# Kernel tuning notes

Hardware: AMD Instinct MI355X
Metric: run time of the kernel (lower is better)

The kernel has to match this reference:

```python
import jax, jax.numpy as jnp
import numpy as np

B, T, C = 4, 128, 512
NH, HS = 8, 64          # n_head, head_dim = C // NH
ORDER = 3               # attention_order
SCALE = 1.0 / np.sqrt(HS)


def setup_inputs() -> dict:
    key = jax.random.key(0)
    ks = jax.random.split(key, 7)
    s = 0.02
    return {
        "x": jax.random.normal(ks[0], (B, T, C), jnp.float32),
        "Wp0": jax.random.normal(ks[1], (C, C), jnp.float32) * s,
        "Wp1": jax.random.normal(ks[2], (C, C), jnp.float32) * s,
        "Wp2": jax.random.normal(ks[3], (C, C), jnp.float32) * s,
        "Wv0": jax.random.normal(ks[4], (HS, HS), jnp.float32) * s,
        "Wv1": jax.random.normal(ks[5], (HS, HS), jnp.float32) * s,
        "Wc": jax.random.normal(ks[6], (C, C), jnp.float32) * s,
    }


def _heads(x, W):
    # Linear then split heads: (B,T,C) -> (B,NH,T,HS)
    return (x @ W).reshape(B, T, NH, HS).transpose(0, 2, 1, 3)


def _causal_mask(t, order):
    # indices grid [T]^order, True where i0 >= i1 >= ... >= i_{order-1}
    idx = jnp.arange(t)
    g = jnp.stack(jnp.meshgrid(*([idx] * order), indexing='ij'), axis=-1)
    return jnp.all(jnp.diff(g, axis=-1) <= 0, axis=-1)


def reference(x, Wp0, Wp1, Wp2, Wv0, Wv1, Wc):
    p0 = _heads(x, Wp0)  # (B,NH,T,HS)
    p1 = _heads(x, Wp1)
    p2 = _heads(x, Wp2)

    # pairwise scores, then higher-order broadcast exactly as the torch einsum
    # ('bh...i,bhkd->bh...ik' sums the key over d and broadcasts — faithful).
    att = jnp.einsum('bhid,bhjd->bhij', p0, p1) * SCALE        # (B,NH,T,T)
    att = jnp.einsum('bh...i,bhkd->bh...ik', att, p2)          # (B,NH,T,T,T)

    mask = _causal_mask(T, ORDER)[None, None]                  # (1,1,T,T,T)
    att = jnp.where(mask, att, -jnp.inf)
    att = jax.nn.softmax(att.reshape(B, NH, T, T * T), axis=-1)

    # value tensors with broadcasted elementwise product over the order dims
    V0 = (p1 @ Wv0)[:, :, :, None, :]   # (B,NH,T,1,HS)
    V1 = (p2 @ Wv1)[:, :, None, :, :]   # (B,NH,1,T,HS)
    V = (V0 * V1).reshape(B, NH, T * T, HS)

    y = jnp.einsum('bhij,bhjd->bhid', att, V)                  # (B,NH,T,HS)
    y = y.transpose(0, 2, 1, 3).reshape(B, T, C)
    return y @ Wc
```

## Files before the change

### kernel.cpp

```cpp
#include <hip/hip_runtime.h>
#include <hip/hip_bf16.h>
#include <math.h>

#define B 4
#define T 128
#define C 512
#define NH 8
#define HS 64
#define BH (B*NH)

typedef __attribute__((ext_vector_type(8))) short bf16x8;
typedef __attribute__((ext_vector_type(4))) float f32x4;

__device__ __forceinline__ unsigned short bfc(float x) {
    return __builtin_bit_cast(unsigned short, __float2bfloat16(x));
}
__device__ __forceinline__ float b2f(unsigned short u) {
    unsigned int x = ((unsigned int)u) << 16;
    return __builtin_bit_cast(float, x);
}
__device__ __forceinline__ unsigned int pk_bf16(float a, float b) {
    return (unsigned int)bfc(a) | ((unsigned int)bfc(b) << 16);
}
__device__ __forceinline__ float lo_f(unsigned int g) {
    return __builtin_bit_cast(float, g << 16);
}
__device__ __forceinline__ float hi_f(unsigned int g) {
    return __builtin_bit_cast(float, g & 0xffff0000u);
}

__global__ __launch_bounds__(256) void prep_kernel(
    const float* __restrict__ X, const float* __restrict__ Wp0, const float* __restrict__ Wp1,
    const float* __restrict__ Wp2, const float* __restrict__ Wc,
    const float* __restrict__ Wv0, const float* __restrict__ Wv1,
    unsigned short* __restrict__ Xb, unsigned short* __restrict__ W0T, unsigned short* __restrict__ W1T,
    unsigned short* __restrict__ W2T, unsigned short* __restrict__ WcT,
    unsigned short* __restrict__ We0T, unsigned short* __restrict__ We1T)
{
    __shared__ float Ls[64][69];
    __shared__ float As[16][68];
    __shared__ float Bs[16][68];
    const int z = blockIdx.z;
    const int tid = threadIdx.x;
    if (z == 0) {
        const int r0 = blockIdx.y * 64, c0 = blockIdx.x * 64;
        #pragma unroll
        for (int it = 0; it < 2; ++it) {
            const int q = tid + it * 256;
            const int row = q >> 3, c8 = (q & 7) * 8;
            const float4 a = *(const float4*)&X[(size_t)(r0 + row) * 512 + c0 + c8];
            const float4 b = *(const float4*)&X[(size_t)(r0 + row) * 512 + c0 + c8 + 4];
            uint4 o;
            o.x = pk_bf16(a.x, a.y);
            o.y = pk_bf16(a.z, a.w);
            o.z = pk_bf16(b.x, b.y);
            o.w = pk_bf16(b.z, b.w);
            *(uint4*)&Xb[(size_t)(r0 + row) * 512 + c0 + c8] = o;
        }
        return;
    }
    if (z <= 4) {
        const int r0 = blockIdx.y * 64, c0 = blockIdx.x * 64;
        const float* W = (z == 1) ? Wp0 : (z == 2) ? Wp1 : (z == 3) ? Wp2 : Wc;
        unsigned short* WT = (z == 1) ? W0T : (z == 2) ? W1T : (z == 3) ? W2T : WcT;
        #pragma unroll
        for (int it = 0; it < 4; ++it) {
            const int q = tid + it * 256;
            const int row = q >> 4, c4 = (q & 15) * 4;
            const float4 v = *(const float4*)&W[(size_t)(r0 + row) * 512 + c0 + c4];
            Ls[row][c4 + 0] = v.x; Ls[row][c4 + 1] = v.y; Ls[row][c4 + 2] = v.z; Ls[row][c4 + 3] = v.w;
        }
        __syncthreads();
        #pragma unroll
        for (int it = 0; it < 2; ++it) {
            const int q = tid + it * 256;
            const int nrow = q >> 3, k8 = (q & 7) * 8;
            uint4 o;
            o.x = pk_bf16(Ls[k8 + 0][nrow], Ls[k8 + 1][nrow]);
            o.y = pk_bf16(Ls[k8 + 2][nrow], Ls[k8 + 3][nrow]);
            o.z = pk_bf16(Ls[k8 + 4][nrow], Ls[k8 + 5][nrow]);
            o.w = pk_bf16(Ls[k8 + 6][nrow], Ls[k8 + 7][nrow]);
            *(uint4*)&WT[(size_t)(c0 + nrow) * 512 + r0 + k8] = o;
        }
        return;
    }
    const float* A  = (z == 5) ? Wp1 : Wp2;
    const float* Wv = (z == 5) ? Wv0 : Wv1;
    unsigned short* O = (z == 5) ? We0T : We1T;
    const int h = blockIdx.x;
    const int m0 = blockIdx.y * 64;
    const int tx = tid & 15, ty = tid >> 4;
    const int arow = tid >> 2, acol = (tid & 3) * 4;
    const int brow = tid >> 4, bcol = (tid & 15) * 4;
    float acc[4][4] = {};
    for (int k0 = 0; k0 < 64; k0 += 16) {
        const float4 av = *(const float4*)&A[(size_t)(m0 + arow) * 512 + h * 64 + k0 + acol];
        const float4 bv = *(const float4*)&Wv[(size_t)(k0 + brow) * 64 + bcol];
        __syncthreads();
        As[acol + 0][arow] = av.x; As[acol + 1][arow] = av.y;
        As[acol + 2][arow] = av.z; As[acol + 3][arow] = av.w;
        *(float4*)&Bs[brow][bcol] = bv;
        __syncthreads();
        #pragma unroll
        for (int kk = 0; kk < 16; ++kk) {
            const float4 a4 = *(const float4*)&As[kk][ty * 4];
            const float4 b4 = *(const float4*)&Bs[kk][tx * 4];
            const float ar[4] = {a4.x, a4.y, a4.z, a4.w};
            const float br[4] = {b4.x, b4.y, b4.z, b4.w};
            #pragma unroll
            for (int r = 0; r < 4; ++r)
                #pragma unroll
                for (int c = 0; c < 4; ++c)
                    acc[r][c] = fmaf(ar[r], br[c], acc[r][c]);
        }
    }
    #pragma unroll
    for (int r = 0; r < 4; ++r)
        #pragma unroll
        for (int c = 0; c < 4; ++c)
            O[(size_t)(h * 64 + tx * 4 + c) * 512 + (m0 + ty * 4 + r)] = bfc(acc[r][c]);
}

__global__ __launch_bounds__(256) void projmm_kernel(
    const unsigned short* __restrict__ Xb,
    const unsigned short* __restrict__ W0T, const unsigned short* __restrict__ W1T,
    const unsigned short* __restrict__ W2T,
    const unsigned short* __restrict__ We0T, const unsigned short* __restrict__ We1T,
    unsigned short* __restrict__ p0b, unsigned short* __restrict__ p1b,
    unsigned short* __restrict__ V0T, unsigned short* __restrict__ V1T, float* __restrict__ rr)
{
    __shared__ __align__(16) unsigned short As[64][72];
    __shared__ __align__(16) unsigned short Bs[64][72];
    __shared__ float sRS[4][64];
    const int z = blockIdx.z;
    const unsigned short* WT = (z == 0) ? W0T : (z == 1) ? W1T : (z == 2) ? W2T : (z == 3) ? We0T : We1T;
    const int m0 = blockIdx.y * 64, n0 = blockIdx.x * 64;
    const int tid = threadIdx.x;
    const int w = tid >> 6, lane = tid & 63, quad = lane >> 4, l16 = lane & 15;
    f32x4 acc[4];
    #pragma unroll
    for (int mt = 0; mt < 4; ++mt) acc[mt] = (f32x4){0.f, 0.f, 0.f, 0.f};
    for (int k0 = 0; k0 < 512; k0 += 64) {
        __syncthreads();
        #pragma unroll
        for (int it = 0; it < 2; ++it) {
            const int q = tid + it * 256;
            const int row = q >> 3, c8 = (q & 7) * 8;
            *(uint4*)&As[row][c8] = *(const uint4*)&Xb[(size_t)(m0 + row) * 512 + k0 + c8];
            *(uint4*)&Bs[row][c8] = *(const uint4*)&WT[(size_t)(n0 + row) * 512 + k0 + c8];
        }
        __syncthreads();
        #pragma unroll
        for (int kt = 0; kt < 2; ++kt) {
            const bf16x8 b8 = *(const bf16x8*)&Bs[w * 16 + l16][kt * 32 + quad * 8];
            #pragma unroll
            for (int mt = 0; mt < 4; ++mt) {
                const bf16x8 a8 = *(const bf16x8*)&As[mt * 16 + l16][kt * 32 + quad * 8];
                acc[mt] = __builtin_amdgcn_mfma_f32_16x16x32_bf16(a8, b8, acc[mt], 0, 0, 0);
            }
        }
    }
    if (z == 2) {
        #pragma unroll
        for (int mt = 0; mt < 4; ++mt)
            #pragma unroll
            for (int r = 0; r < 4; ++r) {
                float v = acc[mt][r];
                v += __shfl_xor(v, 1, 64); v += __shfl_xor(v, 2, 64);
                v += __shfl_xor(v, 4, 64); v += __shfl_xor(v, 8, 64);
                if (l16 == 0) sRS[w][mt * 16 + quad * 4 + r] = v;
            }
        __syncthreads();
        if (tid < 64) {
            const float s = sRS[0][tid] + sRS[1][tid] + sRS[2][tid] + sRS[3][tid];
            const int m = m0 + tid, b = m >> 7, tl = m & 127, h = n0 >> 6;
            rr[(b * NH + h) * T + tl] = s;
        }
        return;
    }
    const int n = n0 + w * 16 + l16;
    const int h = n >> 6, d = n & 63;
    #pragma unroll
    for (int mt = 0; mt < 4; ++mt) {
        #pragma unroll
        for (int r = 0; r < 4; ++r) {
            const int m = m0 + mt * 16 + quad * 4 + r;
            const int b = m >> 7, t = m & 127;
            const size_t hm = (size_t)(b * NH + h) * T + t;
            const float v = acc[mt][r];
            if (z == 0)      p0b[hm * HS + d] = bfc(v);
            else if (z == 1) p1b[hm * HS + d] = bfc(v);
            else if (z == 3) V0T[((size_t)(b * NH + h) * HS + d) * T + t] = bfc(v);
            else             V1T[((size_t)(b * NH + h) * HS + d) * T + t] = bfc(v);
        }
    }
}

__global__ __launch_bounds__(256) void attn_kernel(
    const unsigned short* __restrict__ p0b, const unsigned short* __restrict__ p1b,
    const float* __restrict__ rr, const unsigned short* __restrict__ V0Tg,
    const unsigned short* __restrict__ V1Tg, unsigned short* __restrict__ Yb)
{
    __shared__ __align__(16) unsigned short sE[128 * 64];
    __shared__ float sS[8][128];
    __shared__ float srr[128];
    __shared__ float sZ[4];

    const int bid = blockIdx.x;
    const int bh = bid & (BH - 1);
    const int ig = bid >> 5;
    const int tid = threadIdx.x;
    const int w = tid >> 6;
    const int lane = tid & 63;
    const int quad = lane >> 4;
    const int l16 = lane & 15;

    if (tid < 128) srr[tid] = rr[bh * T + tid];

    uint4 v1r[4];
    {
        const unsigned short* src = V1Tg + ((size_t)bh * HS + (w << 4) + l16) * T + (quad << 3);
        #pragma unroll
        for (int kt = 0; kt < 4; ++kt) v1r[kt] = *(const uint4*)(src + (kt << 5));
    }

    {
        const int qr = l16 & 7;
        const int irow = (qr & 1) ? (16 * qr + 15 - ig) : (16 * qr + ig);
        const unsigned short* ap = p0b + ((size_t)bh * T + irow) * HS + (quad << 3);
        const unsigned short* bp = p1b + (size_t)bh * T * HS + (quad << 3);
        f32x4 s0 = (f32x4){0.f, 0.f, 0.f, 0.f};
        f32x4 s1 = (f32x4){0.f, 0.f, 0.f, 0.f};
        #pragma unroll
        for (int kt = 0; kt < 2; ++kt) {
            const bf16x8 a8 = *(const bf16x8*)(ap + (kt << 5));
            const bf16x8 b0 = *(const bf16x8*)(bp + (size_t)((w << 5) + l16) * HS + (kt << 5));
            const bf16x8 b1 = *(const bf16x8*)(bp + (size_t)((w << 5) + 16 + l16) * HS + (kt << 5));
            s0 = __builtin_amdgcn_mfma_f32_16x16x32_bf16(a8, b0, s0, 0, 0, 0);
            s1 = __builtin_amdgcn_mfma_f32_16x16x32_bf16(a8, b1, s1, 0, 0, 0);
        }
        if (quad < 2) {
            #pragma unroll
            for (int r = 0; r < 4; ++r) {
                sS[quad * 4 + r][(w << 5) + l16]      = s0[r] * 0.125f;
                sS[quad * 4 + r][(w << 5) + 16 + l16] = s1[r] * 0.125f;
            }
        }
    }
    __syncthreads();

    const unsigned short* v0t = V0Tg + ((size_t)bh * HS + (w << 4) + l16) * T;
    const float L2E = 1.4426950408889634f;

    for (int qq = 7; qq >= 0; --qq) {
        const int i = (qq & 1) ? (16 * qq + 15 - ig) : (16 * qq + ig);
        const float* sSq = sS[qq];

        float mhat;
        {
            float a0 = (lane <= i) ? fabsf(sSq[lane]) : 0.f;
            float a1 = (64 + lane <= i) ? fabsf(sSq[64 + lane]) : 0.f;
            float r0 = (lane <= i) ? fabsf(srr[lane]) : 0.f;
            float r1 = (64 + lane <= i) ? fabsf(srr[64 + lane]) : 0.f;
            float aS = fmaxf(a0, a1), aR = fmaxf(r0, r1);
            #pragma unroll
            for (int off = 32; off; off >>= 1) {
                aS = fmaxf(aS, __shfl_xor(aS, off, 64));
                aR = fmaxf(aR, __shfl_xor(aR, off, 64));
            }
            mhat = aS * aR;
        }

        const float bexp = -mhat * L2E;
        const int mtmax = i >> 4;
        const int cc = tid & 7;
        const int rowin = tid >> 3;
        const int k0l = cc << 3;
        float zacc = 0.f;

        float rk[8];
        *(float4*)&rk[0] = *(const float4*)&srr[k0l];
        *(float4*)&rk[4] = *(const float4*)&srr[k0l + 4];
        const int npass0 = (mtmax >> 1) + 1;
        for (int p = 0; p < npass0; ++p) {
            const int jj = (p << 5) + rowin;
            uint4 o = {0u, 0u, 0u, 0u};
            if (jj <= i && k0l <= jj) {
                const float aL = sSq[jj] * L2E;
                const int dlim = jj - k0l;
                float e[8];
                #pragma unroll
                for (int q = 0; q < 8; ++q) {
                    const float ex = __builtin_amdgcn_exp2f(fmaf(aL, rk[q], bexp));
                    e[q] = (q <= dlim) ? ex : 0.f;
                    zacc += e[q];
                }
                o.x = pk_bf16(e[0], e[1]);
                o.y = pk_bf16(e[2], e[3]);
                o.z = pk_bf16(e[4], e[5]);
                o.w = pk_bf16(e[6], e[7]);
            }
            *(uint4*)&sE[(jj << 6) + ((cc ^ (jj & 7)) << 3)] = o;
        }

        f32x4 acc[8];
        #pragma unroll
        for (int mt = 0; mt < 8; ++mt) acc[mt] = (f32x4){0.f, 0.f, 0.f, 0.f};

        if (mtmax < 4) {
            #pragma unroll
            for (int off = 32; off; off >>= 1) zacc += __shfl_xor(zacc, off, 64);
            if (lane == 0) sZ[w] = zacc;
            __syncthreads();
            #pragma unroll
            for (int mt = 0; mt < 4; ++mt) {
                if (mt <= mtmax) {
                    #pragma unroll
                    for (int kt = 0; kt <= 1; ++kt) {
                        if (kt <= (mt >> 1)) {
                            const int swz = ((kt << 2) + quad) ^ (l16 & 7);
                            const bf16x8 a8 = *(const bf16x8*)&sE[(((mt << 4) + l16) << 6) + (swz << 3)];
                            acc[mt] = __builtin_amdgcn_mfma_f32_16x16x32_bf16(
                                a8, __builtin_bit_cast(bf16x8, v1r[kt]), acc[mt], 0, 0, 0);
                        }
                    }
                }
            }
        } else {
            __syncthreads();
            #pragma unroll
            for (int mt = 0; mt < 8; ++mt) {
                if (mt <= mtmax) {
                    #pragma unroll
                    for (int kt = 0; kt <= 1; ++kt) {
                        if (kt <= (mt >> 1)) {
                            const int swz = ((kt << 2) + quad) ^ (l16 & 7);
                            const bf16x8 a8 = *(const bf16x8*)&sE[(((mt << 4) + l16) << 6) + (swz << 3)];
                            acc[mt] = __builtin_amdgcn_mfma_f32_16x16x32_bf16(
                                a8, __builtin_bit_cast(bf16x8, v1r[kt]), acc[mt], 0, 0, 0);
                        }
                    }
                }
            }
            __syncthreads();
            *(float4*)&rk[0] = *(const float4*)&srr[64 + k0l];
            *(float4*)&rk[4] = *(const float4*)&srr[64 + k0l + 4];
            const int npass1 = ((mtmax - 4) >> 1) + 1;
            for (int p = 0; p < npass1; ++p) {
                const int jj = 64 + (p << 5) + rowin;
                uint4 o = {0u, 0u, 0u, 0u};
                if (jj <= i && 64 + k0l <= jj) {
                    const float aL = sSq[jj] * L2E;
                    const int dlim = jj - 64 - k0l;
                    float e[8];
                    #pragma unroll
                    for (int q = 0; q < 8; ++q) {
                        const float ex = __builtin_amdgcn_exp2f(fmaf(aL, rk[q], bexp));
                        e[q] = (q <= dlim) ? ex : 0.f;
                        zacc += e[q];
                    }
                    o.x = pk_bf16(e[0], e[1]);
                    o.y = pk_bf16(e[2], e[3]);
                    o.z = pk_bf16(e[4], e[5]);
                    o.w = pk_bf16(e[6], e[7]);
                }
                *(uint4*)&sE[(jj << 6) + ((cc ^ (jj & 7)) << 3)] = o;
            }
            #pragma unroll
            for (int off = 32; off; off >>= 1) zacc += __shfl_xor(zacc, off, 64);
            if (lane == 0) sZ[w] = zacc;
            __syncthreads();
            #pragma unroll
            for (int mt = 4; mt < 8; ++mt) {
                if (mt <= mtmax) {
                    #pragma unroll
                    for (int kt = 2; kt <= 3; ++kt) {
                        if (kt <= (mt >> 1)) {
                            const int swz = (((kt & 1) << 2) + quad) ^ (l16 & 7);
                            const bf16x8 a8 = *(const bf16x8*)&sE[(((mt << 4) + l16) << 6) + (swz << 3)];
                            acc[mt] = __builtin_amdgcn_mfma_f32_16x16x32_bf16(
                                a8, __builtin_bit_cast(bf16x8, v1r[kt]), acc[mt], 0, 0, 0);
                        }
                    }
                }
            }
        }
        const float Z = sZ[0] + sZ[1] + sZ[2] + sZ[3];

        float part = 0.f;
        #pragma unroll
        for (int mt = 0; mt < 8; ++mt) {
            if (mt < mtmax) {
                const uint2 u = *(const uint2*)&v0t[(mt << 4) + (quad << 2)];
                part = fmaf(lo_f(u.x), acc[mt][0], part);
                part = fmaf(hi_f(u.x), acc[mt][1], part);
                part = fmaf(lo_f(u.y), acc[mt][2], part);
                part = fmaf(hi_f(u.y), acc[mt][3], part);
            } else if (mt == mtmax) {
                const uint2 u = *(const uint2*)&v0t[(mt << 4) + (quad << 2)];
                const int jb = (mt << 4) + (quad << 2);
                if (jb + 0 <= i) part = fmaf(lo_f(u.x), acc[mt][0], part);
                if (jb + 1 <= i) part = fmaf(hi_f(u.x), acc[mt][1], part);
                if (jb + 2 <= i) part = fmaf(lo_f(u.y), acc[mt][2], part);
                if (jb + 3 <= i) part = fmaf(hi_f(u.y), acc[mt][3], part);
            }
        }
        part += __shfl_xor(part, 16, 64);
        part += __shfl_xor(part, 32, 64);
        if (lane < 16) {
            const int bb = bh >> 3, hh = bh & 7;
            Yb[((size_t)(bb * T + i) * C) + hh * HS + (w << 4) + l16] = bfc(part / Z);
        }
        __syncthreads();
    }
}

__global__ __launch_bounds__(256) void outmm_kernel(
    const unsigned short* __restrict__ Ab, const unsigned short* __restrict__ WT,
    float* __restrict__ OUT)
{
    __shared__ __align__(16) unsigned short As[64][72];
    __shared__ __align__(16) unsigned short Bs[64][72];
    const int m0 = blockIdx.y * 64, n0 = blockIdx.x * 64;
    const int tid = threadIdx.x;
    const int w = tid >> 6, lane = tid & 63, quad = lane >> 4, l16 = lane & 15;
    f32x4 acc[4];
    #pragma unroll
    for (int mt = 0; mt < 4; ++mt) acc[mt] = (f32x4){0.f, 0.f, 0.f, 0.f};
    for (int k0 = 0; k0 < 512; k0 += 64) {
        __syncthreads();
        #pragma unroll
        for (int it = 0; it < 2; ++it) {
            const int q = tid + it * 256;
            const int row = q >> 3, c8 = (q & 7) * 8;
            *(uint4*)&As[row][c8] = *(const uint4*)&Ab[(size_t)(m0 + row) * 512 + k0 + c8];
            *(uint4*)&Bs[row][c8] = *(const uint4*)&WT[(size_t)(n0 + row) * 512 + k0 + c8];
        }
        __syncthreads();
        #pragma unroll
        for (int kt = 0; kt < 2; ++kt) {
            const bf16x8 b8 = *(const bf16x8*)&Bs[w * 16 + l16][kt * 32 + quad * 8];
            #pragma unroll
            for (int mt = 0; mt < 4; ++mt) {
                const bf16x8 a8 = *(const bf16x8*)&As[mt * 16 + l16][kt * 32 + quad * 8];
                acc[mt] = __builtin_amdgcn_mfma_f32_16x16x32_bf16(a8, b8, acc[mt], 0, 0, 0);
            }
        }
    }
    const int n = n0 + w * 16 + l16;
    #pragma unroll
    for (int mt = 0; mt < 4; ++mt)
        #pragma unroll
        for (int r = 0; r < 4; ++r) {
            const int mrow = m0 + mt * 16 + quad * 4 + r;
            OUT[(size_t)mrow * 512 + n] = acc[mt][r];
        }
}

extern "C" void kernel_launch(void* const* d_in, const int* in_sizes, int n_in,
                              void* d_out, int out_size, void* d_ws, size_t ws_size,
                              hipStream_t stream)
{
    const float* x   = (const float*)d_in[0];
    const float* Wp0 = (const float*)d_in[1];
    const float* Wp1 = (const float*)d_in[2];
    const float* Wp2 = (const float*)d_in[3];
    const float* Wv0 = (const float*)d_in[4];
    const float* Wv1 = (const float*)d_in[5];
    const float* Wc  = (const float*)d_in[6];
    float* out = (float*)d_out;

    char* w8 = (char*)d_ws;
    const size_t HB = 512 * 1024;
    unsigned short* Xb   = (unsigned short*)(w8 + 0 * HB);
    unsigned short* W0T  = (unsigned short*)(w8 + 1 * HB);
    unsigned short* W1T  = (unsigned short*)(w8 + 2 * HB);
    unsigned short* W2T  = (unsigned short*)(w8 + 3 * HB);
    unsigned short* WcT  = (unsigned short*)(w8 + 4 * HB);
    unsigned short* We0T = (unsigned short*)(w8 + 5 * HB);
    unsigned short* We1T = (unsigned short*)(w8 + 6 * HB);
    unsigned short* p0b  = (unsigned short*)(w8 + 7 * HB);
    unsigned short* p1b  = (unsigned short*)(w8 + 8 * HB);
    unsigned short* V0T  = (unsigned short*)(w8 + 9 * HB);
    unsigned short* V1T  = (unsigned short*)(w8 + 10 * HB);
    unsigned short* Yb   = (unsigned short*)(w8 + 11 * HB);
    float*          rr   = (float*)        (w8 + 12 * HB);

    prep_kernel  <<<dim3(8, 8, 7), 256, 0, stream>>>(x, Wp0, Wp1, Wp2, Wc, Wv0, Wv1,
                                                     Xb, W0T, W1T, W2T, WcT, We0T, We1T);
    projmm_kernel<<<dim3(8, 8, 5), 256, 0, stream>>>(Xb, W0T, W1T, W2T, We0T, We1T,
                                                     p0b, p1b, V0T, V1T, rr);
    attn_kernel  <<<dim3(512), 256, 0, stream>>>(p0b, p1b, rr, V0T, V1T, Yb);
    outmm_kernel <<<dim3(8, 8), 256, 0, stream>>>(Yb, WcT, out);
}
```

Measured before the change: 120.9 us.

## Fuse fp32-to-bf16 conversion into GEMMs and compute value projections inside attention

Removes the separate prep kernel: the projection and output GEMMs now load fp32 X and weights directly, converting and transposing them in shared memory per tile. The Wv value projections are no longer folded into the big GEMM. Instead each attention block computes V0/V1 from p1/p2 with MFMA into shared memory, unioned with the existing score buffers. This cuts one launch and the global round-trips for bf16 copies, at the cost of redundant per-tile weight conversion and extra per-block work in attention.

```diff
diff --git a/kernel.cpp b/kernel.cpp
--- a/kernel.cpp
+++ b/kernel.cpp
@@ -15,10 +15,6 @@
 __device__ __forceinline__ unsigned short bfc(float x) {
     return __builtin_bit_cast(unsigned short, __float2bfloat16(x));
 }
-__device__ __forceinline__ float b2f(unsigned short u) {
-    unsigned int x = ((unsigned int)u) << 16;
-    return __builtin_bit_cast(float, x);
-}
 __device__ __forceinline__ unsigned int pk_bf16(float a, float b) {
     return (unsigned int)bfc(a) | ((unsigned int)bfc(b) << 16);
 }
@@ -29,46 +25,47 @@
     return __builtin_bit_cast(float, g & 0xffff0000u);
 }
 
-__global__ __launch_bounds__(256) void prep_kernel(
-    const float* __restrict__ X, const float* __restrict__ Wp0, const float* __restrict__ Wp1,
-    const float* __restrict__ Wp2, const float* __restrict__ Wc,
-    const float* __restrict__ Wv0, const float* __restrict__ Wv1,
-    unsigned short* __restrict__ Xb, unsigned short* __restrict__ W0T, unsigned short* __restrict__ W1T,
-    unsigned short* __restrict__ W2T, unsigned short* __restrict__ WcT,
-    unsigned short* __restrict__ We0T, unsigned short* __restrict__ We1T)
+__global__ __launch_bounds__(256) void proj_kernel(
+    const float* __restrict__ X,
+    const float* __restrict__ Wp0, const float* __restrict__ Wp1, const float* __restrict__ Wp2,
+    unsigned short* __restrict__ p0b, unsigned short* __restrict__ p1b,
+    unsigned short* __restrict__ p2b, float* __restrict__ rr)
 {
+    __shared__ __align__(16) unsigned short As[64][72];
+    __shared__ __align__(16) unsigned short Bs[64][72];
     __shared__ float Ls[64][69];
-    __shared__ float As[16][68];
-    __shared__ float Bs[16][68];
+    __shared__ float sRS[4][64];
     const int z = blockIdx.z;
+    const float* W = (z == 0) ? Wp0 : (z == 1) ? Wp1 : Wp2;
+    const int m0 = blockIdx.y * 64, n0 = blockIdx.x * 64;
     const int tid = threadIdx.x;
-    if (z == 0) {
-        const int r0 = blockIdx.y * 64, c0 = blockIdx.x * 64;
+    const int w = tid >> 6, lane = tid & 63, quad = lane >> 4, l16 = lane & 15;
+    f32x4 acc[4];
+    #pragma unroll
+    for (int mt = 0; mt < 4; ++mt) acc[mt] = (f32x4){0.f, 0.f, 0.f, 0.f};
+
+    for (int k0 = 0; k0 < 512; k0 += 64) {
+        __syncthreads();
         #pragma unroll
         for (int it = 0; it < 2; ++it) {
             const int q = tid + it * 256;
             const int row = q >> 3, c8 = (q & 7) * 8;
-            const float4 a = *(const float4*)&X[(size_t)(r0 + row) * 512 + c0 + c8];
-            const float4 b = *(const float4*)&X[(size_t)(r0 + row) * 512 + c0 + c8 + 4];
+            const float4 a = *(const float4*)&X[(size_t)(m0 + row) * 512 + k0 + c8];
+            const float4 b = *(const float4*)&X[(size_t)(m0 + row) * 512 + k0 + c8 + 4];
             uint4 o;
             o.x = pk_bf16(a.x, a.y);
             o.y = pk_bf16(a.z, a.w);
             o.z = pk_bf16(b.x, b.y);
             o.w = pk_bf16(b.z, b.w);
-            *(uint4*)&Xb[(size_t)(r0 + row) * 512 + c0 + c8] = o;
-        }
-        return;
-    }
-    if (z <= 4) {
-        const int r0 = blockIdx.y * 64, c0 = blockIdx.x * 64;
-        const float* W = (z == 1) ? Wp0 : (z == 2) ? Wp1 : (z == 3) ? Wp2 : Wc;
-        unsigned short* WT = (z == 1) ? W0T : (z == 2) ? W1T : (z == 3) ? W2T : WcT;
+            *(uint4*)&As[row][c8] = o;
+        }
         #pragma unroll
         for (int it = 0; it < 4; ++it) {
             const int q = tid + it * 256;
             const int row = q >> 4, c4 = (q & 15) * 4;
-            const float4 v = *(const float4*)&W[(size_t)(r0 + row) * 512 + c0 + c4];
-            Ls[row][c4 + 0] = v.x; Ls[row][c4 + 1] = v.y; Ls[row][c4 + 2] = v.z; Ls[row][c4 + 3] = v.w;
+            const float4 v = *(const float4*)&W[(size_t)(k0 + row) * 512 + n0 + c4];
+            Ls[row][c4 + 0] = v.x; Ls[row][c4 + 1] = v.y;
+            Ls[row][c4 + 2] = v.z; Ls[row][c4 + 3] = v.w;
         }
         __syncthreads();
         #pragma unroll
@@ -80,74 +77,7 @@
             o.y = pk_bf16(Ls[k8 + 2][nrow], Ls[k8 + 3][nrow]);
             o.z = pk_bf16(Ls[k8 + 4][nrow], Ls[k8 + 5][nrow]);
             o.w = pk_bf16(Ls[k8 + 6][nrow], Ls[k8 + 7][nrow]);
-            *(uint4*)&WT[(size_t)(c0 + nrow) * 512 + r0 + k8] = o;
-        }
-        return;
-    }
-    const float* A  = (z == 5) ? Wp1 : Wp2;
-    const float* Wv = (z == 5) ? Wv0 : Wv1;
-    unsigned short* O = (z == 5) ? We0T : We1T;
-    const int h = blockIdx.x;
-    const int m0 = blockIdx.y * 64;
-    const int tx = tid & 15, ty = tid >> 4;
-    const int arow = tid >> 2, acol = (tid & 3) * 4;
-    const int brow = tid >> 4, bcol = (tid & 15) * 4;
-    float acc[4][4] = {};
-    for (int k0 = 0; k0 < 64; k0 += 16) {
-        const float4 av = *(const float4*)&A[(size_t)(m0 + arow) * 512 + h * 64 + k0 + acol];
-        const float4 bv = *(const float4*)&Wv[(size_t)(k0 + brow) * 64 + bcol];
-        __syncthreads();
-        As[acol + 0][arow] = av.x; As[acol + 1][arow] = av.y;
-        As[acol + 2][arow] = av.z; As[acol + 3][arow] = av.w;
-        *(float4*)&Bs[brow][bcol] = bv;
-        __syncthreads();
-        #pragma unroll
-        for (int kk = 0; kk < 16; ++kk) {
-            const float4 a4 = *(const float4*)&As[kk][ty * 4];
-            const float4 b4 = *(const float4*)&Bs[kk][tx * 4];
-            const float ar[4] = {a4.x, a4.y, a4.z, a4.w};
-            const float br[4] = {b4.x, b4.y, b4.z, b4.w};
-            #pragma unroll
-            for (int r = 0; r < 4; ++r)
-                #pragma unroll
-                for (int c = 0; c < 4; ++c)
-                    acc[r][c] = fmaf(ar[r], br[c], acc[r][c]);
-        }
-    }
-    #pragma unroll
-    for (int r = 0; r < 4; ++r)
-        #pragma unroll
-        for (int c = 0; c < 4; ++c)
-            O[(size_t)(h * 64 + tx * 4 + c) * 512 + (m0 + ty * 4 + r)] = bfc(acc[r][c]);
-}
-
-__global__ __launch_bounds__(256) void projmm_kernel(
-    const unsigned short* __restrict__ Xb,
-    const unsigned short* __restrict__ W0T, const unsigned short* __restrict__ W1T,
-    const unsigned short* __restrict__ W2T,
-    const unsigned short* __restrict__ We0T, const unsigned short* __restrict__ We1T,
-    unsigned short* __restrict__ p0b, unsigned short* __restrict__ p1b,
-    unsigned short* __restrict__ V0T, unsigned short* __restrict__ V1T, float* __restrict__ rr)
-{
-    __shared__ __align__(16) unsigned short As[64][72];
-    __shared__ __align__(16) unsigned short Bs[64][72];
-    __shared__ float sRS[4][64];
-    const int z = blockIdx.z;
-    const unsigned short* WT = (z == 0) ? W0T : (z == 1) ? W1T : (z == 2) ? W2T : (z == 3) ? We0T : We1T;
-    const int m0 = blockIdx.y * 64, n0 = blockIdx.x * 64;
-    const int tid = threadIdx.x;
-    const int w = tid >> 6, lane = tid & 63, quad = lane >> 4, l16 = lane & 15;
-    f32x4 acc[4];
-    #pragma unroll
-    for (int mt = 0; mt < 4; ++mt) acc[mt] = (f32x4){0.f, 0.f, 0.f, 0.f};
-    for (int k0 = 0; k0 < 512; k0 += 64) {
-        __syncthreads();
-        #pragma unroll
-        for (int it = 0; it < 2; ++it) {
-            const int q = tid + it * 256;
-            const int row = q >> 3, c8 = (q & 7) * 8;
-            *(uint4*)&As[row][c8] = *(const uint4*)&Xb[(size_t)(m0 + row) * 512 + k0 + c8];
-            *(uint4*)&Bs[row][c8] = *(const uint4*)&WT[(size_t)(n0 + row) * 512 + k0 + c8];
+            *(uint4*)&Bs[nrow][k8] = o;
         }
         __syncthreads();
         #pragma unroll
@@ -157,6 +87,21 @@
             for (int mt = 0; mt < 4; ++mt) {
                 const bf16x8 a8 = *(const bf16x8*)&As[mt * 16 + l16][kt * 32 + quad * 8];
                 acc[mt] = __builtin_amdgcn_mfma_f32_16x16x32_bf16(a8, b8, acc[mt], 0, 0, 0);
+            }
+        }
+    }
+
+    {
+        const int n = n0 + w * 16 + l16;
+        const int h = n >> 6, d = n & 63;
+        unsigned short* pz = (z == 0) ? p0b : (z == 1) ? p1b : p2b;
+        #pragma unroll
+        for (int mt = 0; mt < 4; ++mt) {
+            #pragma unroll
+            for (int r = 0; r < 4; ++r) {
+                const int m = m0 + mt * 16 + quad * 4 + r;
+                const int bb = m >> 7, t = m & 127;
+                pz[((size_t)(bb * NH + h) * T + t) * HS + d] = bfc(acc[mt][r]);
             }
         }
     }
@@ -173,36 +118,24 @@
         __syncthreads();
         if (tid < 64) {
             const float s = sRS[0][tid] + sRS[1][tid] + sRS[2][tid] + sRS[3][tid];
-            const int m = m0 + tid, b = m >> 7, tl = m & 127, h = n0 >> 6;
-            rr[(b * NH + h) * T + tl] = s;
-        }
-        return;
-    }
-    const int n = n0 + w * 16 + l16;
-    const int h = n >> 6, d = n & 63;
-    #pragma unroll
-    for (int mt = 0; mt < 4; ++mt) {
-        #pragma unroll
-        for (int r = 0; r < 4; ++r) {
-            const int m = m0 + mt * 16 + quad * 4 + r;
-            const int b = m >> 7, t = m & 127;
-            const size_t hm = (size_t)(b * NH + h) * T + t;
-            const float v = acc[mt][r];
-            if (z == 0)      p0b[hm * HS + d] = bfc(v);
-            else if (z == 1) p1b[hm * HS + d] = bfc(v);
-            else if (z == 3) V0T[((size_t)(b * NH + h) * HS + d) * T + t] = bfc(v);
-            else             V1T[((size_t)(b * NH + h) * HS + d) * T + t] = bfc(v);
+            const int m = m0 + tid, bb = m >> 7, tl = m & 127, h = n0 >> 6;
+            rr[(bb * NH + h) * T + tl] = s;
         }
     }
 }
 
 __global__ __launch_bounds__(256) void attn_kernel(
     const unsigned short* __restrict__ p0b, const unsigned short* __restrict__ p1b,
-    const float* __restrict__ rr, const unsigned short* __restrict__ V0Tg,
-    const unsigned short* __restrict__ V1Tg, unsigned short* __restrict__ Yb)
+    const unsigned short* __restrict__ p2b, const float* __restrict__ rr,
+    const float* __restrict__ Wv0, const float* __restrict__ Wv1,
+    unsigned short* __restrict__ Yb)
 {
-    __shared__ __align__(16) unsigned short sE[128 * 64];
-    __shared__ float sS[8][128];
+    __shared__ __align__(16) unsigned short sV0T[64][136];
+    __shared__ __align__(16) unsigned short sV1T[64][136];
+    __shared__ __align__(16) union {
+        unsigned short sWvT[2][64][72];
+        struct { unsigned short sE[128 * 64]; float sS[8][128]; } e;
+    } u;
     __shared__ float srr[128];
     __shared__ float sZ[4];
 
@@ -217,12 +150,54 @@
 
     if (tid < 128) srr[tid] = rr[bh * T + tid];
 
+    #pragma unroll
+    for (int v = 0; v < 2; ++v) {
+        const float* Wv = v ? Wv1 : Wv0;
+        #pragma unroll
+        for (int it = 0; it < 4; ++it) {
+            const int k = (tid >> 4) + it * 16;
+            const int d0 = (tid & 15) * 4;
+            const float4 wv = *(const float4*)&Wv[(size_t)k * 64 + d0];
+            u.sWvT[v][d0 + 0][k] = bfc(wv.x);
+            u.sWvT[v][d0 + 1][k] = bfc(wv.y);
+            u.sWvT[v][d0 + 2][k] = bfc(wv.z);
+            u.sWvT[v][d0 + 3][k] = bfc(wv.w);
+        }
+    }
+    __syncthreads();
+
+    #pragma unroll
+    for (int v = 0; v < 2; ++v) {
+        const unsigned short* pg = v ? p2b : p1b;
+        unsigned short (*dst)[136] = v ? sV1T : sV0T;
+        #pragma unroll
+        for (int nn = 0; nn < 2; ++nn) {
+            const int nt = w + nn * 4;
+            f32x4 vacc[4];
+            #pragma unroll
+            for (int mt = 0; mt < 4; ++mt) vacc[mt] = (f32x4){0.f, 0.f, 0.f, 0.f};
+            #pragma unroll
+            for (int kt = 0; kt < 2; ++kt) {
+                const bf16x8 b8 = *(const bf16x8*)&pg[((size_t)bh * T + nt * 16 + l16) * HS + kt * 32 + quad * 8];
+                #pragma unroll
+                for (int mt = 0; mt < 4; ++mt) {
+                    const bf16x8 a8 = *(const bf16x8*)&u.sWvT[v][mt * 16 + l16][kt * 32 + quad * 8];
+                    vacc[mt] = __builtin_amdgcn_mfma_f32_16x16x32_bf16(a8, b8, vacc[mt], 0, 0, 0);
+                }
+            }
+            #pragma unroll
+            for (int mt = 0; mt < 4; ++mt)
+                #pragma unroll
+                for (int r = 0; r < 4; ++r)
+                    dst[mt * 16 + quad * 4 + r][nt * 16 + l16] = bfc(vacc[mt][r]);
+        }
+    }
+    __syncthreads();
+
     uint4 v1r[4];
-    {
-        const unsigned short* src = V1Tg + ((size_t)bh * HS + (w << 4) + l16) * T + (quad << 3);
-        #pragma unroll
-        for (int kt = 0; kt < 4; ++kt) v1r[kt] = *(const uint4*)(src + (kt << 5));
-    }
+    #pragma unroll
+    for (int kt = 0; kt < 4; ++kt)
+        v1r[kt] = *(const uint4*)&sV1T[(w << 4) + l16][(quad << 3) + (kt << 5)];
 
     {
         const int qr = l16 & 7;
@@ -242,19 +217,18 @@
         if (quad < 2) {
             #pragma unroll
             for (int r = 0; r < 4; ++r) {
-                sS[quad * 4 + r][(w << 5) + l16]      = s0[r] * 0.125f;
-                sS[quad * 4 + r][(w << 5) + 16 + l16] = s1[r] * 0.125f;
+                u.e.sS[quad * 4 + r][(w << 5) + l16]      = s0[r] * 0.125f;
+                u.e.sS[quad * 4 + r][(w << 5) + 16 + l16] = s1[r] * 0.125f;
             }
         }
     }
     __syncthreads();
 
-    const unsigned short* v0t = V0Tg + ((size_t)bh * HS + (w << 4) + l16) * T;
     const float L2E = 1.4426950408889634f;
 
     for (int qq = 7; qq >= 0; --qq) {
         const int i = (qq & 1) ? (16 * qq + 15 - ig) : (16 * qq + ig);
-        const float* sSq = sS[qq];
+        const float* sSq = u.e.sS[qq];
 
         float mhat;
         {
@@ -300,7 +274,7 @@
                 o.z = pk_bf16(e[4], e[5]);
                 o.w = pk_bf16(e[6], e[7]);
             }
-            *(uint4*)&sE[(jj << 6) + ((cc ^ (jj & 7)) << 3)] = o;
+            *(uint4*)&u.e.sE[(jj << 6) + ((cc ^ (jj & 7)) << 3)] = o;
         }
 
         f32x4 acc[8];
@@ -319,7 +293,7 @@
                     for (int kt = 0; kt <= 1; ++kt) {
                         if (kt <= (mt >> 1)) {
                             const int swz = ((kt << 2) + quad) ^ (l16 & 7);
-                            const bf16x8 a8 = *(const bf16x8*)&sE[(((mt << 4) + l16) << 6) + (swz << 3)];
+                            const bf16x8 a8 = *(const bf16x8*)&u.e.sE[(((mt << 4) + l16) << 6) + (swz << 3)];
                             acc[mt] = __builtin_amdgcn_mfma_f32_16x16x32_bf16(
                                 a8, __builtin_bit_cast(bf16x8, v1r[kt]), acc[mt], 0, 0, 0);
                         }
@@ -335,7 +309,7 @@
                     for (int kt = 0; kt <= 1; ++kt) {
                         if (kt <= (mt >> 1)) {
                             const int swz = ((kt << 2) + quad) ^ (l16 & 7);
-                            const bf16x8 a8 = *(const bf16x8*)&sE[(((mt << 4) + l16) << 6) + (swz << 3)];
+                            const bf16x8 a8 = *(const bf16x8*)&u.e.sE[(((mt << 4) + l16) << 6) + (swz << 3)];
                             acc[mt] = __builtin_amdgcn_mfma_f32_16x16x32_bf16(
                                 a8, __builtin_bit_cast(bf16x8, v1r[kt]), acc[mt], 0, 0, 0);
                         }
@@ -364,7 +338,7 @@
                     o.z = pk_bf16(e[4], e[5]);
                     o.w = pk_bf16(e[6], e[7]);
                 }
-                *(uint4*)&sE[(jj << 6) + ((cc ^ (jj & 7)) << 3)] = o;
+                *(uint4*)&u.e.sE[(jj << 6) + ((cc ^ (jj & 7)) << 3)] = o;
             }
             #pragma unroll
             for (int off = 32; off; off >>= 1) zacc += __shfl_xor(zacc, off, 64);
@@ -377,7 +351,7 @@
                     for (int kt = 2; kt <= 3; ++kt) {
                         if (kt <= (mt >> 1)) {
                             const int swz = (((kt & 1) << 2) + quad) ^ (l16 & 7);
-                            const bf16x8 a8 = *(const bf16x8*)&sE[(((mt << 4) + l16) << 6) + (swz << 3)];
+                            const bf16x8 a8 = *(const bf16x8*)&u.e.sE[(((mt << 4) + l16) << 6) + (swz << 3)];
                             acc[mt] = __builtin_amdgcn_mfma_f32_16x16x32_bf16(
                                 a8, __builtin_bit_cast(bf16x8, v1r[kt]), acc[mt], 0, 0, 0);
                         }
@@ -387,22 +361,23 @@
         }
         const float Z = sZ[0] + sZ[1] + sZ[2] + sZ[3];
 
+        const unsigned short* v0row = sV0T[(w << 4) + l16];
         float part = 0.f;
         #pragma unroll
         for (int mt = 0; mt < 8; ++mt) {
             if (mt < mtmax) {
-                const uint2 u = *(const uint2*)&v0t[(mt << 4) + (quad << 2)];
-                part = fmaf(lo_f(u.x), acc[mt][0], part);
-                part = fmaf(hi_f(u.x), acc[mt][1], part);
-                part = fmaf(lo_f(u.y), acc[mt][2], part);
-                part = fmaf(hi_f(u.y), acc[mt][3], part);
+                const uint2 uu = *(const uint2*)&v0row[(mt << 4) + (quad << 2)];
+                part = fmaf(lo_f(uu.x), acc[mt][0], part);
+                part = fmaf(hi_f(uu.x), acc[mt][1], part);
+                part = fmaf(lo_f(uu.y), acc[mt][2], part);
+                part = fmaf(hi_f(uu.y), acc[mt][3], part);
             } else if (mt == mtmax) {
-                const uint2 u = *(const uint2*)&v0t[(mt << 4) + (quad << 2)];
+                const uint2 uu = *(const uint2*)&v0row[(mt << 4) + (quad << 2)];
                 const int jb = (mt << 4) + (quad << 2);
-                if (jb + 0 <= i) part = fmaf(lo_f(u.x), acc[mt][0], part);
-                if (jb + 1 <= i) part = fmaf(hi_f(u.x), acc[mt][1], part);
-                if (jb + 2 <= i) part = fmaf(lo_f(u.y), acc[mt][2], part);
-                if (jb + 3 <= i) part = fmaf(hi_f(u.y), acc[mt][3], part);
+                if (jb + 0 <= i) part = fmaf(lo_f(uu.x), acc[mt][0], part);
+                if (jb + 1 <= i) part = fmaf(hi_f(uu.x), acc[mt][1], part);
+                if (jb + 2 <= i) part = fmaf(lo_f(uu.y), acc[mt][2], part);
+                if (jb + 3 <= i) part = fmaf(hi_f(uu.y), acc[mt][3], part);
             }
         }
         part += __shfl_xor(part, 16, 64);
@@ -416,11 +391,12 @@
 }
 
 __global__ __launch_bounds__(256) void outmm_kernel(
-    const unsigned short* __restrict__ Ab, const unsigned short* __restrict__ WT,
+    const unsigned short* __restrict__ Ab, const float* __restrict__ Wc,
     float* __restrict__ OUT)
 {
     __shared__ __align__(16) unsigned short As[64][72];
     __shared__ __align__(16) unsigned short Bs[64][72];
+    __shared__ float Ls[64][69];
     const int m0 = blockIdx.y * 64, n0 = blockIdx.x * 64;
     const int tid = threadIdx.x;
     const int w = tid >> 6, lane = tid & 63, quad = lane >> 4, l16 = lane & 15;
@@ -434,7 +410,26 @@
             const int q = tid + it * 256;
             const int row = q >> 3, c8 = (q & 7) * 8;
             *(uint4*)&As[row][c8] = *(const uint4*)&Ab[(size_t)(m0 + row) * 512 + k0 + c8];
-            *(uint4*)&Bs[row][c8] = *(const uint4*)&WT[(size_t)(n0 + row) * 512 + k0 + c8];
+        }
+        #pragma unroll
+        for (int it = 0; it < 4; ++it) {
+            const int q = tid + it * 256;
+            const int row = q >> 4, c4 = (q & 15) * 4;
+            const float4 v = *(const float4*)&Wc[(size_t)(k0 + row) * 512 + n0 + c4];
+            Ls[row][c4 + 0] = v.x; Ls[row][c4 + 1] = v.y;
+            Ls[row][c4 + 2] = v.z; Ls[row][c4 + 3] = v.w;
+        }
+        __syncthreads();
+        #pragma unroll
+        for (int it = 0; it < 2; ++it) {
+            const int q = tid + it * 256;
+            const int nrow = q >> 3, k8 = (q & 7) * 8;
+            uint4 o;
+            o.x = pk_bf16(Ls[k8 + 0][nrow], Ls[k8 + 1][nrow]);
+            o.y = pk_bf16(Ls[k8 + 2][nrow], Ls[k8 + 3][nrow]);
+            o.z = pk_bf16(Ls[k8 + 4][nrow], Ls[k8 + 5][nrow]);
+            o.w = pk_bf16(Ls[k8 + 6][nrow], Ls[k8 + 7][nrow]);
+            *(uint4*)&Bs[nrow][k8] = o;
         }
         __syncthreads();
         #pragma unroll
@@ -472,24 +467,13 @@
 
     char* w8 = (char*)d_ws;
     const size_t HB = 512 * 1024;
-    unsigned short* Xb   = (unsigned short*)(w8 + 0 * HB);
-    unsigned short* W0T  = (unsigned short*)(w8 + 1 * HB);
-    unsigned short* W1T  = (unsigned short*)(w8 + 2 * HB);
-    unsigned short* W2T  = (unsigned short*)(w8 + 3 * HB);
-    unsigned short* WcT  = (unsigned short*)(w8 + 4 * HB);
-    unsigned short* We0T = (unsigned short*)(w8 + 5 * HB);
-    unsigned short* We1T = (unsigned short*)(w8 + 6 * HB);
-    unsigned short* p0b  = (unsigned short*)(w8 + 7 * HB);
-    unsigned short* p1b  = (unsigned short*)(w8 + 8 * HB);
-    unsigned short* V0T  = (unsigned short*)(w8 + 9 * HB);
-    unsigned short* V1T  = (unsigned short*)(w8 + 10 * HB);
-    unsigned short* Yb   = (unsigned short*)(w8 + 11 * HB);
-    float*          rr   = (float*)        (w8 + 12 * HB);
-
-    prep_kernel  <<<dim3(8, 8, 7), 256, 0, stream>>>(x, Wp0, Wp1, Wp2, Wc, Wv0, Wv1,
-                                                     Xb, W0T, W1T, W2T, WcT, We0T, We1T);
-    projmm_kernel<<<dim3(8, 8, 5), 256, 0, stream>>>(Xb, W0T, W1T, W2T, We0T, We1T,
-                                                     p0b, p1b, V0T, V1T, rr);
-    attn_kernel  <<<dim3(512), 256, 0, stream>>>(p0b, p1b, rr, V0T, V1T, Yb);
-    outmm_kernel <<<dim3(8, 8), 256, 0, stream>>>(Yb, WcT, out);
-}
+    unsigned short* p0b = (unsigned short*)(w8 + 0 * HB);
+    unsigned short* p1b = (unsigned short*)(w8 + 1 * HB);
+    unsigned short* p2b = (unsigned short*)(w8 + 2 * HB);
+    unsigned short* Yb  = (unsigned short*)(w8 + 3 * HB);
+    float*          rr  = (float*)        (w8 + 4 * HB);
+
+    proj_kernel <<<dim3(8, 8, 3), 256, 0, stream>>>(x, Wp0, Wp1, Wp2, p0b, p1b, p2b, rr);
+    attn_kernel <<<dim3(512), 256, 0, stream>>>(p0b, p1b, p2b, rr, Wv0, Wv1, Yb);
+    outmm_kernel<<<dim3(8, 8), 256, 0, stream>>>(Yb, Wc, out);
+}
```

After: 116.4 us. 1.04x faster.
